# Performance work log

Measured on AMD Instinct MI355X. Metric: run time of the kernel, lower is better.

Reference implementation:

```python
import jax, jax.numpy as jnp
import numpy as np

N, D_IN, D_OUT = 4096, 1024, 1024


def setup_inputs() -> dict:
    key = jax.random.key(0)
    kx, kq, kk, kv = jax.random.split(key, 4)
    s = 1.0 / np.sqrt(D_IN)
    return {
        "x": jax.random.normal(kx, (N, D_IN), dtype=jnp.float32),
        "Wq": jax.random.normal(kq, (D_OUT, D_IN), dtype=jnp.float32) * s,
        "Wk": jax.random.normal(kk, (D_OUT, D_IN), dtype=jnp.float32) * s,
        "Wv": jax.random.normal(kv, (D_OUT, D_IN), dtype=jnp.float32) * s,
    }


def reference(x, Wq, Wk, Wv):
    # nn.Linear(d_in, d_out, bias=False): y = x @ W.T with W: [d_out, d_in]
    q = x @ Wq.T            # [N, d_out]
    k = x @ Wk.T            # [N, d_out]
    v = x @ Wv.T            # [N, d_out]
    scores = q @ k.T        # [N, N]
    scale = 1.0 / jnp.sqrt(jnp.asarray(k.shape[-1], dtype=x.dtype))
    attn = jax.nn.softmax(scores * scale, axis=-1)
    return attn @ v         # [N, d_out]
```

## Files before the change

kernel.cpp:

```cpp
#include <hip/hip_runtime.h>


typedef __attribute__((ext_vector_type(8))) __bf16 bf16x8;
typedef __attribute__((ext_vector_type(4))) float floatx4;

#define GLB_AS __attribute__((address_space(1)))
#define LDS_AS __attribute__((address_space(3)))

static __device__ __forceinline__ unsigned short f2bf_u16(float f) {
  union { float f; unsigned u; } x; x.f = f;
  unsigned r = x.u;
  r += 0x7fffu + ((r >> 16) & 1u);
  return (unsigned short)(r >> 16);
}

__global__ __launch_bounds__(256) void cast_f32_bf16(const float* __restrict__ in,
                                                     unsigned short* __restrict__ out) {
  int i = blockIdx.x * 256 + threadIdx.x;
  float4 v = reinterpret_cast<const float4*>(in)[i];
  ushort4 o = make_ushort4(f2bf_u16(v.x), f2bf_u16(v.y), f2bf_u16(v.z), f2bf_u16(v.w));
  reinterpret_cast<ushort4*>(out)[i] = o;
}

__global__ __launch_bounds__(256) void transpose_bf16(const unsigned short* __restrict__ in, int inLd,
                                                      unsigned short* __restrict__ out, int outLd) {
  __shared__ unsigned short tl[32][33];
  const int bi = blockIdx.y, bj = blockIdx.x;
  const int tx = threadIdx.x & 31, ty = threadIdx.x >> 5;
#pragma unroll
  for (int p = 0; p < 4; ++p)
    tl[ty + p * 8][tx] = in[(size_t)(bi * 32 + ty + p * 8) * inLd + bj * 32 + tx];
  __syncthreads();
#pragma unroll
  for (int p = 0; p < 4; ++p)
    out[(size_t)(bj * 32 + ty + p * 8) * outLd + bi * 32 + tx] = tl[tx][ty + p * 8];
}

struct GemmOuts { void* c[4]; int ldc[4]; };

template <int EPI>
__global__ __launch_bounds__(512, 2) void gemm256(const unsigned short* __restrict__ A,
                                                  const unsigned short* __restrict__ B,
                                                  GemmOuts outs, int lda, int ldb,
                                                  int klen, float scale) {
  __shared__ unsigned short sh[65536];
  const int t = threadIdx.x;
  const int w = t >> 6, lane = t & 63;
  const int wm = w >> 2, wn = w & 3;
  const int row0 = blockIdx.y * 256;
  const int col0 = blockIdx.x * 256;
  const int z = blockIdx.z;
  const int kstart = z * klen;
  const int NT = klen >> 6;

  const int scbe = (((t & 3) ^ ((t >> 3) & 3)) << 3);
  const unsigned short* gA0 = A + (size_t)(row0 + (t >> 2)) * lda + kstart + scbe;
  const unsigned short* gA1 = gA0 + (size_t)128 * lda;
  const unsigned short* gB0 = B + (size_t)(col0 + (t >> 2)) * ldb + kstart + scbe;
  const unsigned short* gB1 = gB0 + (size_t)128 * ldb;

#define STAGE_HALF(h_) do { \
    const int tile_ = (h_) >> 2, opb_ = (h_) & 1, kh_ = ((h_) >> 1) & 1; \
    const int lo_ = (((tile_) & 1) << 15) + (opb_ << 14) + (kh_ << 13) + (w << 9); \
    const unsigned short* s0_ = (opb_ ? gB0 : gA0) + tile_ * 64 + kh_ * 32; \
    const unsigned short* s1_ = (opb_ ? gB1 : gA1) + tile_ * 64 + kh_ * 32; \
    __builtin_amdgcn_global_load_lds((const GLB_AS void*)s0_, (LDS_AS void*)&sh[lo_], 16, 0, 0); \
    __builtin_amdgcn_global_load_lds((const GLB_AS void*)s1_, (LDS_AS void*)&sh[lo_ + 4096], 16, 0, 0); \
  } while (0)
#define STAGE_IF(h_) do { const int hh_ = (h_); if (hh_ < 4 * NT) STAGE_HALF(hh_); } while (0)

  const int fr = lane & 15;
  const int sg = (((lane >> 4) ^ ((lane >> 1) & 3)) << 3);
  int aofs[8], bofs[4];
#pragma unroll
  for (int mf = 0; mf < 8; ++mf) aofs[mf] = ((wm * 128 + mf * 16 + fr) << 5) + sg;
#pragma unroll
  for (int nf = 0; nf < 4; ++nf) bofs[nf] = 16384 + ((wn * 64 + nf * 16 + fr) << 5) + sg;

  floatx4 acc[8][4] = {};

#pragma unroll
  for (int h = 0; h < 7; ++h) STAGE_IF(h);
  asm volatile("s_waitcnt vmcnt(6)" ::: "memory");
  __builtin_amdgcn_s_barrier();

  for (int tile = 0; tile < NT; ++tile) {
    const int bo = (tile & 1) << 15;
    bf16x8 a0[8], b0[2], b1[2];

#pragma unroll
    for (int mf = 0; mf < 8; ++mf) a0[mf] = *(const bf16x8*)&sh[bo + aofs[mf]];
    b0[0] = *(const bf16x8*)&sh[bo + bofs[0]];
    b0[1] = *(const bf16x8*)&sh[bo + bofs[1]];
    STAGE_IF(4 * tile + 7);
    __builtin_amdgcn_s_barrier();
    asm volatile("s_waitcnt lgkmcnt(0)" ::: "memory");
    __builtin_amdgcn_sched_barrier(0);
    __builtin_amdgcn_s_setprio(1);
#pragma unroll
    for (int mf = 0; mf < 8; ++mf)
#pragma unroll
      for (int nf = 0; nf < 2; ++nf)
        acc[mf][nf] = __builtin_amdgcn_mfma_f32_16x16x32_bf16(a0[mf], b0[nf], acc[mf][nf], 0, 0, 0);
    __builtin_amdgcn_s_setprio(0);
    __builtin_amdgcn_s_barrier();

    b1[0] = *(const bf16x8*)&sh[bo + bofs[2]];
    b1[1] = *(const bf16x8*)&sh[bo + bofs[3]];
    STAGE_IF(4 * tile + 8);
    __builtin_amdgcn_s_barrier();
    asm volatile("s_waitcnt lgkmcnt(0)" ::: "memory");
    __builtin_amdgcn_sched_barrier(0);
    __builtin_amdgcn_s_setprio(1);
#pragma unroll
    for (int mf = 0; mf < 8; ++mf)
#pragma unroll
      for (int nf = 0; nf < 2; ++nf)
        acc[mf][2 + nf] = __builtin_amdgcn_mfma_f32_16x16x32_bf16(a0[mf], b1[nf], acc[mf][2 + nf], 0, 0, 0);
    __builtin_amdgcn_s_setprio(0);
    __builtin_amdgcn_s_barrier();

#pragma unroll
    for (int mf = 0; mf < 8; ++mf) a0[mf] = *(const bf16x8*)&sh[bo + 8192 + aofs[mf]];
    b0[0] = *(const bf16x8*)&sh[bo + 8192 + bofs[0]];
    b0[1] = *(const bf16x8*)&sh[bo + 8192 + bofs[1]];
    STAGE_IF(4 * tile + 9);
    __builtin_amdgcn_s_barrier();
    asm volatile("s_waitcnt lgkmcnt(0)" ::: "memory");
    __builtin_amdgcn_sched_barrier(0);
    __builtin_amdgcn_s_setprio(1);
#pragma unroll
    for (int mf = 0; mf < 8; ++mf)
#pragma unroll
      for (int nf = 0; nf < 2; ++nf)
        acc[mf][nf] = __builtin_amdgcn_mfma_f32_16x16x32_bf16(a0[mf], b0[nf], acc[mf][nf], 0, 0, 0);
    __builtin_amdgcn_s_setprio(0);
    __builtin_amdgcn_s_barrier();

    b1[0] = *(const bf16x8*)&sh[bo + 8192 + bofs[2]];
    b1[1] = *(const bf16x8*)&sh[bo + 8192 + bofs[3]];
    STAGE_IF(4 * tile + 10);
    __builtin_amdgcn_s_barrier();
    asm volatile("s_waitcnt lgkmcnt(0)" ::: "memory");
    __builtin_amdgcn_sched_barrier(0);
    __builtin_amdgcn_s_setprio(1);
#pragma unroll
    for (int mf = 0; mf < 8; ++mf)
#pragma unroll
      for (int nf = 0; nf < 2; ++nf)
        acc[mf][2 + nf] = __builtin_amdgcn_mfma_f32_16x16x32_bf16(a0[mf], b1[nf], acc[mf][2 + nf], 0, 0, 0);
    __builtin_amdgcn_s_setprio(0);
    if (tile < NT - 2)       { asm volatile("s_waitcnt vmcnt(6)" ::: "memory"); }
    else if (tile == NT - 2) { asm volatile("s_waitcnt vmcnt(0)" ::: "memory"); }
    __builtin_amdgcn_s_barrier();
  }

#undef STAGE_HALF
#undef STAGE_IF

  float* Cf = (float*)outs.c[z];
  unsigned short* Cb = (unsigned short*)outs.c[z];
  const int ldc = outs.ldc[z];
  const int er = (lane >> 4) * 4;
  const int ec = lane & 15;
#pragma unroll
  for (int mf = 0; mf < 8; ++mf)
#pragma unroll
    for (int nf = 0; nf < 4; ++nf)
#pragma unroll
      for (int r = 0; r < 4; ++r) {
        const int m = row0 + wm * 128 + mf * 16 + er + r;
        const int n = col0 + wn * 64 + nf * 16 + ec;
        const float v = acc[mf][nf][r] * scale;
        if (EPI == 0)      Cf[(size_t)m * ldc + n] = v;
        else if (EPI == 1) Cb[(size_t)m * ldc + n] = f2bf_u16(v);
        else               Cb[(size_t)m * ldc + n] = f2bf_u16(__expf(v));
      }
}

static __device__ __forceinline__ float bfpair(unsigned u) {
  union { unsigned u; float f; } a, b;
  a.u = u << 16; b.u = u & 0xffff0000u;
  return a.f + b.f;
}

__global__ __launch_bounds__(256) void rowsum_bf16(const unsigned short* __restrict__ P,
                                                   float* __restrict__ rs) {
  const int w = threadIdx.x >> 6, lane = threadIdx.x & 63;
  const int row = blockIdx.x * 4 + w;
  const uint4* p = (const uint4*)(P + (size_t)row * 4096);
  float s = 0.f;
#pragma unroll
  for (int c = 0; c < 8; ++c) {
    uint4 u = p[c * 64 + lane];
    s += bfpair(u.x) + bfpair(u.y) + bfpair(u.z) + bfpair(u.w);
  }
#pragma unroll
  for (int off = 32; off >= 1; off >>= 1) s += __shfl_xor(s, off);
  if (lane == 0) rs[row] = s;
}

__global__ __launch_bounds__(256) void reduce_pv(float* __restrict__ out,
                                                 const float* __restrict__ p1,
                                                 const float* __restrict__ p2,
                                                 const float* __restrict__ p3,
                                                 const float* __restrict__ rs) {
  const int row = blockIdx.x;
  const int idx = row * 256 + threadIdx.x;
  const float inv = 1.0f / rs[row];
  float4 o = ((const float4*)out)[idx];
  float4 a = ((const float4*)p1)[idx];
  float4 b = ((const float4*)p2)[idx];
  float4 c = ((const float4*)p3)[idx];
  o.x = (o.x + a.x + b.x + c.x) * inv;
  o.y = (o.y + a.y + b.y + c.y) * inv;
  o.z = (o.z + a.z + b.z + c.z) * inv;
  o.w = (o.w + a.w + b.w + c.w) * inv;
  ((float4*)out)[idx] = o;
}

extern "C" void kernel_launch(void* const* d_in, const int* in_sizes, int n_in,
                              void* d_out, int out_size, void* d_ws, size_t ws_size,
                              hipStream_t stream) {
  const float* x  = (const float*)d_in[0];
  const float* Wq = (const float*)d_in[1];
  const float* Wk = (const float*)d_in[2];
  const float* Wv = (const float*)d_in[3];
  float* out = (float*)d_out;

  const int N = 4096, D = 1024;

  char* ws = (char*)d_ws;
  unsigned short* P    = (unsigned short*)ws;
  float*          p1   = (float*)(ws + (32u << 20));
  float*          p2   = (float*)(ws + (48u << 20));
  unsigned short* xb   = (unsigned short*)(ws + (64u << 20));
  unsigned short* wb   = (unsigned short*)(ws + (72u << 20));
  unsigned short* qkvb = (unsigned short*)(ws + (78u << 20));
  float*          p3   = (float*)(ws + (78u << 20));
  float*          rs   = (float*)(ws + (94u << 20));
  unsigned short* vT   = xb;

  cast_f32_bf16<<<N * D / 1024, 256, 0, stream>>>(x, xb);
  cast_f32_bf16<<<D * D / 1024, 256, 0, stream>>>(Wq, wb);
  cast_f32_bf16<<<D * D / 1024, 256, 0, stream>>>(Wk, wb + (size_t)D * D);
  cast_f32_bf16<<<D * D / 1024, 256, 0, stream>>>(Wv, wb + (size_t)2 * D * D);

  GemmOuts oq; oq.c[0] = oq.c[1] = oq.c[2] = oq.c[3] = qkvb;
  oq.ldc[0] = oq.ldc[1] = oq.ldc[2] = oq.ldc[3] = 3 * D;
  gemm256<1><<<dim3(3 * D / 256, N / 256, 1), 512, 0, stream>>>(xb, wb, oq, D, D, D, 1.0f);

  transpose_bf16<<<dim3(D / 32, N / 32), 256, 0, stream>>>(qkvb + 2048, 3 * D, vT, N);

  GemmOuts os; os.c[0] = os.c[1] = os.c[2] = os.c[3] = P;
  os.ldc[0] = os.ldc[1] = os.ldc[2] = os.ldc[3] = N;
  gemm256<2><<<dim3(N / 256, N / 256, 1), 512, 0, stream>>>(qkvb, qkvb + D, os, 3 * D, 3 * D, D, 0.03125f);

  rowsum_bf16<<<N / 4, 256, 0, stream>>>(P, rs);

  GemmOuts op;
  op.c[0] = out; op.ldc[0] = D;
  op.c[1] = p1;  op.ldc[1] = D;
  op.c[2] = p2;  op.ldc[2] = D;
  op.c[3] = p3;  op.ldc[3] = D;
  gemm256<0><<<dim3(D / 256, N / 256, 4), 512, 0, stream>>>(P, vT, op, N, N, N / 4, 1.0f);

  reduce_pv<<<N, 256, 0, stream>>>(out, p1, p2, p3, rs);
}
```

Measured before the change: 160.1 us.

## Fuse casts, V transpose, and row sums into GEMM epilogues; remap block order

The four cast launches become one kernel. The V transpose now happens in the QKV GEMM epilogue, which writes vT directly. Row sums of exp(scores) are computed in the scores GEMM epilogue with shuffles and atomicAdd, replacing the separate rowsum pass. Blocks are remapped with an XCD-style swizzle, and the split-K partials are stored as bf16 instead of fp32, which cuts workspace traffic but adds rounding error and atomic contention.

```diff
diff --git a/kernel.cpp b/kernel.cpp
--- a/kernel.cpp
+++ b/kernel.cpp
@@ -13,27 +13,31 @@
   r += 0x7fffu + ((r >> 16) & 1u);
   return (unsigned short)(r >> 16);
 }
-
-__global__ __launch_bounds__(256) void cast_f32_bf16(const float* __restrict__ in,
-                                                     unsigned short* __restrict__ out) {
-  int i = blockIdx.x * 256 + threadIdx.x;
-  float4 v = reinterpret_cast<const float4*>(in)[i];
+static __device__ __forceinline__ float bf2f(unsigned short u) {
+  union { unsigned u; float f; } x; x.u = ((unsigned)u) << 16; return x.f;
+}
+
+__global__ __launch_bounds__(256) void zero_rs(float* __restrict__ rs) {
+  ((float4*)rs)[blockIdx.x * 256 + threadIdx.x] = make_float4(0.f, 0.f, 0.f, 0.f);
+}
+
+__global__ __launch_bounds__(256) void cast_all(const float* __restrict__ x,
+                                                const float* __restrict__ Wq,
+                                                const float* __restrict__ Wk,
+                                                const float* __restrict__ Wv,
+                                                unsigned short* __restrict__ xb,
+                                                unsigned short* __restrict__ wb) {
+  const int i = blockIdx.x * 256 + threadIdx.x;
+  const int NX4 = 4096 * 1024 / 4;
+  const int NW4 = 1024 * 1024 / 4;
+  const float* src; unsigned short* dst; int k;
+  if (i < NX4)                { src = x;  dst = xb; k = i; }
+  else if (i < NX4 + NW4)     { src = Wq; dst = wb;                 k = i - NX4; }
+  else if (i < NX4 + 2 * NW4) { src = Wk; dst = wb + 1024 * 1024;   k = i - NX4 - NW4; }
+  else                        { src = Wv; dst = wb + 2 * 1024 * 1024; k = i - NX4 - 2 * NW4; }
+  float4 v = reinterpret_cast<const float4*>(src)[k];
   ushort4 o = make_ushort4(f2bf_u16(v.x), f2bf_u16(v.y), f2bf_u16(v.z), f2bf_u16(v.w));
-  reinterpret_cast<ushort4*>(out)[i] = o;
-}
-
-__global__ __launch_bounds__(256) void transpose_bf16(const unsigned short* __restrict__ in, int inLd,
-                                                      unsigned short* __restrict__ out, int outLd) {
-  __shared__ unsigned short tl[32][33];
-  const int bi = blockIdx.y, bj = blockIdx.x;
-  const int tx = threadIdx.x & 31, ty = threadIdx.x >> 5;
-#pragma unroll
-  for (int p = 0; p < 4; ++p)
-    tl[ty + p * 8][tx] = in[(size_t)(bi * 32 + ty + p * 8) * inLd + bj * 32 + tx];
-  __syncthreads();
-#pragma unroll
-  for (int p = 0; p < 4; ++p)
-    out[(size_t)(bj * 32 + ty + p * 8) * outLd + bi * 32 + tx] = tl[tx][ty + p * 8];
+  reinterpret_cast<ushort4*>(dst)[k] = o;
 }
 
 struct GemmOuts { void* c[4]; int ldc[4]; };
@@ -47,8 +51,12 @@
   const int t = threadIdx.x;
   const int w = t >> 6, lane = t & 63;
   const int wm = w >> 2, wn = w & 3;
-  const int row0 = blockIdx.y * 256;
-  const int col0 = blockIdx.x * 256;
+  const int gx = gridDim.x;
+  const int nwg = gx * gridDim.y;
+  int bid = blockIdx.y * gx + blockIdx.x;
+  bid = (bid & 7) * (nwg >> 3) + (bid >> 3);
+  const int row0 = (bid / gx) * 256;
+  const int col0 = (bid % gx) * 256;
   const int z = blockIdx.z;
   const int kstart = z * klen;
   const int NT = klen >> 6;
@@ -158,64 +166,101 @@
 #undef STAGE_HALF
 #undef STAGE_IF
 
-  float* Cf = (float*)outs.c[z];
-  unsigned short* Cb = (unsigned short*)outs.c[z];
-  const int ldc = outs.ldc[z];
   const int er = (lane >> 4) * 4;
   const int ec = lane & 15;
-#pragma unroll
-  for (int mf = 0; mf < 8; ++mf)
-#pragma unroll
-    for (int nf = 0; nf < 4; ++nf)
+
+  if (EPI == 0) {
+    if (z == 0) {
+      float* Cf = (float*)outs.c[0];
+      const int ldc = outs.ldc[0];
+#pragma unroll
+      for (int mf = 0; mf < 8; ++mf)
+#pragma unroll
+        for (int nf = 0; nf < 4; ++nf)
+#pragma unroll
+          for (int r = 0; r < 4; ++r)
+            Cf[(size_t)(row0 + wm * 128 + mf * 16 + er + r) * ldc +
+               (col0 + wn * 64 + nf * 16 + ec)] = acc[mf][nf][r] * scale;
+    } else {
+      unsigned short* Cb = (unsigned short*)outs.c[z];
+      const int ldc = outs.ldc[z];
+#pragma unroll
+      for (int mf = 0; mf < 8; ++mf)
+#pragma unroll
+        for (int nf = 0; nf < 4; ++nf)
+#pragma unroll
+          for (int r = 0; r < 4; ++r)
+            Cb[(size_t)(row0 + wm * 128 + mf * 16 + er + r) * ldc +
+               (col0 + wn * 64 + nf * 16 + ec)] = f2bf_u16(acc[mf][nf][r] * scale);
+    }
+  } else if (EPI == 2) {
+    unsigned short* Pb = (unsigned short*)outs.c[0];
+    float* rsp = (float*)outs.c[1];
+    const int ldc = outs.ldc[0];
+#pragma unroll
+    for (int mf = 0; mf < 8; ++mf) {
 #pragma unroll
       for (int r = 0; r < 4; ++r) {
         const int m = row0 + wm * 128 + mf * 16 + er + r;
-        const int n = col0 + wn * 64 + nf * 16 + ec;
-        const float v = acc[mf][nf][r] * scale;
-        if (EPI == 0)      Cf[(size_t)m * ldc + n] = v;
-        else if (EPI == 1) Cb[(size_t)m * ldc + n] = f2bf_u16(v);
-        else               Cb[(size_t)m * ldc + n] = f2bf_u16(__expf(v));
+        float rsum = 0.f;
+#pragma unroll
+        for (int nf = 0; nf < 4; ++nf) {
+          const float e = __expf(acc[mf][nf][r] * scale);
+          Pb[(size_t)m * ldc + (col0 + wn * 64 + nf * 16 + ec)] = f2bf_u16(e);
+          rsum += e;
+        }
+        rsum += __shfl_xor(rsum, 1);
+        rsum += __shfl_xor(rsum, 2);
+        rsum += __shfl_xor(rsum, 4);
+        rsum += __shfl_xor(rsum, 8);
+        if (ec == 0) atomicAdd(rsp + m, rsum);
       }
-}
-
-static __device__ __forceinline__ float bfpair(unsigned u) {
-  union { unsigned u; float f; } a, b;
-  a.u = u << 16; b.u = u & 0xffff0000u;
-  return a.f + b.f;
-}
-
-__global__ __launch_bounds__(256) void rowsum_bf16(const unsigned short* __restrict__ P,
-                                                   float* __restrict__ rs) {
-  const int w = threadIdx.x >> 6, lane = threadIdx.x & 63;
-  const int row = blockIdx.x * 4 + w;
-  const uint4* p = (const uint4*)(P + (size_t)row * 4096);
-  float s = 0.f;
-#pragma unroll
-  for (int c = 0; c < 8; ++c) {
-    uint4 u = p[c * 64 + lane];
-    s += bfpair(u.x) + bfpair(u.y) + bfpair(u.z) + bfpair(u.w);
+    }
+  } else {
+    if (col0 < 2048) {
+      unsigned short* qkb = (unsigned short*)outs.c[0];
+#pragma unroll
+      for (int mf = 0; mf < 8; ++mf)
+#pragma unroll
+        for (int nf = 0; nf < 4; ++nf)
+#pragma unroll
+          for (int r = 0; r < 4; ++r)
+            qkb[(size_t)(row0 + wm * 128 + mf * 16 + er + r) * 2048 +
+                (col0 + wn * 64 + nf * 16 + ec)] = f2bf_u16(acc[mf][nf][r] * scale);
+    } else {
+      unsigned short* vT = (unsigned short*)outs.c[1];
+#pragma unroll
+      for (int mf = 0; mf < 8; ++mf)
+#pragma unroll
+        for (int nf = 0; nf < 4; ++nf) {
+          const int n = (col0 - 2048) + wn * 64 + nf * 16 + ec;
+          const int mb = row0 + wm * 128 + mf * 16 + er;
+          ushort4 o = make_ushort4(f2bf_u16(acc[mf][nf][0] * scale),
+                                   f2bf_u16(acc[mf][nf][1] * scale),
+                                   f2bf_u16(acc[mf][nf][2] * scale),
+                                   f2bf_u16(acc[mf][nf][3] * scale));
+          *reinterpret_cast<ushort4*>(&vT[(size_t)n * 4096 + mb]) = o;
+        }
+    }
   }
-#pragma unroll
-  for (int off = 32; off >= 1; off >>= 1) s += __shfl_xor(s, off);
-  if (lane == 0) rs[row] = s;
 }
 
 __global__ __launch_bounds__(256) void reduce_pv(float* __restrict__ out,
-                                                 const float* __restrict__ p1,
-                                                 const float* __restrict__ p2,
-                                                 const float* __restrict__ p3,
+                                                 const unsigned short* __restrict__ p1,
+                                                 const unsigned short* __restrict__ p2,
+                                                 const unsigned short* __restrict__ p3,
                                                  const float* __restrict__ rs) {
   const int row = blockIdx.x;
   const int idx = row * 256 + threadIdx.x;
   const float inv = 1.0f / rs[row];
   float4 o = ((const float4*)out)[idx];
-  float4 a = ((const float4*)p1)[idx];
-  float4 b = ((const float4*)p2)[idx];
-  float4 c = ((const float4*)p3)[idx];
-  o.x = (o.x + a.x + b.x + c.x) * inv;
-  o.y = (o.y + a.y + b.y + c.y) * inv;
-  o.z = (o.z + a.z + b.z + c.z) * inv;
-  o.w = (o.w + a.w + b.w + c.w) * inv;
+  ushort4 a = ((const ushort4*)p1)[idx];
+  ushort4 b = ((const ushort4*)p2)[idx];
+  ushort4 c = ((const ushort4*)p3)[idx];
+  o.x = (o.x + bf2f(a.x) + bf2f(b.x) + bf2f(c.x)) * inv;
+  o.y = (o.y + bf2f(a.y) + bf2f(b.y) + bf2f(c.y)) * inv;
+  o.z = (o.z + bf2f(a.z) + bf2f(b.z) + bf2f(c.z)) * inv;
+  o.w = (o.w + bf2f(a.w) + bf2f(b.w) + bf2f(c.w)) * inv;
   ((float4*)out)[idx] = o;
 }
 
@@ -231,32 +276,27 @@
   const int N = 4096, D = 1024;
 
   char* ws = (char*)d_ws;
-  unsigned short* P    = (unsigned short*)ws;
-  float*          p1   = (float*)(ws + (32u << 20));
-  float*          p2   = (float*)(ws + (48u << 20));
-  unsigned short* xb   = (unsigned short*)(ws + (64u << 20));
-  unsigned short* wb   = (unsigned short*)(ws + (72u << 20));
-  unsigned short* qkvb = (unsigned short*)(ws + (78u << 20));
-  float*          p3   = (float*)(ws + (78u << 20));
-  float*          rs   = (float*)(ws + (94u << 20));
-  unsigned short* vT   = xb;
-
-  cast_f32_bf16<<<N * D / 1024, 256, 0, stream>>>(x, xb);
-  cast_f32_bf16<<<D * D / 1024, 256, 0, stream>>>(Wq, wb);
-  cast_f32_bf16<<<D * D / 1024, 256, 0, stream>>>(Wk, wb + (size_t)D * D);
-  cast_f32_bf16<<<D * D / 1024, 256, 0, stream>>>(Wv, wb + (size_t)2 * D * D);
-
-  GemmOuts oq; oq.c[0] = oq.c[1] = oq.c[2] = oq.c[3] = qkvb;
-  oq.ldc[0] = oq.ldc[1] = oq.ldc[2] = oq.ldc[3] = 3 * D;
-  gemm256<1><<<dim3(3 * D / 256, N / 256, 1), 512, 0, stream>>>(xb, wb, oq, D, D, D, 1.0f);
-
-  transpose_bf16<<<dim3(D / 32, N / 32), 256, 0, stream>>>(qkvb + 2048, 3 * D, vT, N);
-
-  GemmOuts os; os.c[0] = os.c[1] = os.c[2] = os.c[3] = P;
-  os.ldc[0] = os.ldc[1] = os.ldc[2] = os.ldc[3] = N;
-  gemm256<2><<<dim3(N / 256, N / 256, 1), 512, 0, stream>>>(qkvb, qkvb + D, os, 3 * D, 3 * D, D, 0.03125f);
-
-  rowsum_bf16<<<N / 4, 256, 0, stream>>>(P, rs);
+  unsigned short* P   = (unsigned short*)ws;
+  unsigned short* qkb = (unsigned short*)(ws + (32u << 20));
+  unsigned short* vT  = (unsigned short*)(ws + (48u << 20));
+  unsigned short* xb  = (unsigned short*)(ws + (56u << 20));
+  unsigned short* wb  = (unsigned short*)(ws + (64u << 20));
+  float*          rs  = (float*)(ws + (70u << 20));
+  unsigned short* p1  = (unsigned short*)(ws + (72u << 20));
+  unsigned short* p2  = (unsigned short*)(ws + (80u << 20));
+  unsigned short* p3  = (unsigned short*)(ws + (88u << 20));
+
+  zero_rs<<<4, 256, 0, stream>>>(rs);
+
+  cast_all<<<7168, 256, 0, stream>>>(x, Wq, Wk, Wv, xb, wb);
+
+  GemmOuts oq; oq.c[0] = qkb; oq.c[1] = vT; oq.c[2] = oq.c[3] = qkb;
+  oq.ldc[0] = 2048; oq.ldc[1] = 4096; oq.ldc[2] = oq.ldc[3] = 2048;
+  gemm256<3><<<dim3(3 * D / 256, N / 256, 1), 512, 0, stream>>>(xb, wb, oq, D, D, D, 1.0f);
+
+  GemmOuts os; os.c[0] = P; os.c[1] = rs; os.c[2] = os.c[3] = P;
+  os.ldc[0] = N; os.ldc[1] = 0; os.ldc[2] = os.ldc[3] = N;
+  gemm256<2><<<dim3(N / 256, N / 256, 1), 512, 0, stream>>>(qkb, qkb + D, os, 2 * D, 2 * D, D, 0.03125f);
 
   GemmOuts op;
   op.c[0] = out; op.ldc[0] = D;
```

Measured after the change: 150.4 us. 1.06x faster.
